# Kernel optimization log

Measured on AMD Instinct MI355X. Metric: run time of the kernel, lower is better.

Reference implementation:

```python
import jax, jax.numpy as jnp
import numpy as np
from jax import lax

# Norse default LIF/LI parameters with dt=0.001
DT_TAU_MEM = 0.1   # dt * tau_mem_inv (1/1e-2)
DT_TAU_SYN = 0.2   # dt * tau_syn_inv (1/5e-3)
V_TH = 0.5
ALPHA = 100.0      # SuperSpike surrogate slope (backward only)

@jax.custom_vjp
def spike(x):
    return (x > 0).astype(x.dtype)

def _spike_fwd(x):
    return (x > 0).astype(x.dtype), x

def _spike_bwd(x, g):
    # SuperSpike surrogate gradient: 1 / (alpha*|x| + 1)^2
    sg = 1.0 / (ALPHA * jnp.abs(x) + 1.0) ** 2
    return (g * sg,)

spike.defvjp(_spike_fwd, _spike_bwd)

def setup_inputs() -> dict:
    key = jax.random.key(0)
    k1, k2, k3 = jax.random.split(key, 3)
    T, B, C, H, W = 64, 512, 1, 28, 28
    IN, HID, OUT = 784, 2048, 10
    x = jax.random.normal(k1, (T, B, C, H, W), dtype=jnp.float32)
    # Kaiming-uniform-ish bias-free Linear weights, torch layout [out, in]
    w1 = jax.random.uniform(k2, (HID, IN), jnp.float32, -1.0, 1.0) / np.sqrt(IN)
    w_out = jax.random.uniform(k3, (OUT, HID), jnp.float32, -1.0, 1.0) / np.sqrt(HID)
    return {"x": x, "w1": w1, "w_out": w_out}

def reference(x, w1, w_out):
    T, B = x.shape[0], x.shape[1]
    HID, OUT = w1.shape[0], w_out.shape[0]
    xf = x.reshape(T, B, -1)  # [T, B, IN]

    def step(carry, xt):
        v1, i1, vo, io = carry
        cur = xt @ w1.T                       # fc1: [B, HID]
        # LIF: decay, threshold/spike/reset, then integrate new input current
        v1_dec = v1 + DT_TAU_MEM * (-v1 + i1)
        i1_dec = i1 * (1.0 - DT_TAU_SYN)
        z = spike(v1_dec - V_TH)
        v1_new = (1.0 - z) * v1_dec           # v_reset = 0
        i1_new = i1_dec + cur
        out_cur = z @ w_out.T                 # fc_out: [B, OUT]
        # LI readout: leaky integration (no spiking)
        vo_new = vo + DT_TAU_MEM * (-vo + io)
        io_new = io * (1.0 - DT_TAU_SYN) + out_cur
        return (v1_new, i1_new, vo_new, io_new), vo_new

    zh = jnp.zeros((B, HID), x.dtype)
    zo = jnp.zeros((B, OUT), x.dtype)
    _, voltages = lax.scan(step, (zh, zh, zo, zo), xf)  # [T, B, OUT]
    return jnp.max(voltages, axis=0)
```

## Files before the change

kernel.cpp:

```cpp
#include <hip/hip_runtime.h>
#include <cstdint>
#include <cstddef>

#define T_STEPS 64
#define BATCH 512
#define IN_F 784
#define KP 800
#define HID 2048
#define OUT_F 10

#define DEC_V 0.9f
#define DEC_I 0.8f
#define DT_V 0.1f
#define V_TH 0.5f

typedef __attribute__((ext_vector_type(8))) _Float16 f16x8;
typedef __attribute__((ext_vector_type(4))) float f32x4;

__device__ __forceinline__ void load_lds16(const _Float16* g, _Float16* l) {
  __builtin_amdgcn_global_load_lds(
      (const __attribute__((address_space(1))) void*)g,
      (__attribute__((address_space(3))) void*)l, 16, 0, 0);
}

__global__ __launch_bounds__(256)
void split_rows(const float* __restrict__ src, _Float16* __restrict__ hi,
                _Float16* __restrict__ lo) {
  const int row = blockIdx.x;
  for (int k = threadIdx.x; k < KP; k += 256) {
    float v = (k < IN_F) ? src[(size_t)row * IN_F + k] : 0.0f;
    _Float16 h = (_Float16)v;
    hi[(size_t)row * KP + k] = h;
    lo[(size_t)row * KP + k] = (_Float16)(v - (float)h);
  }
}

__global__ __launch_bounds__(256)
void pad_wo(const float* __restrict__ wo, _Float16* __restrict__ woF) {
  const int i = blockIdx.x * 256 + threadIdx.x;
  if (i >= 16 * HID) return;
  const int o = i / HID;
  woF[i] = (o < OUT_F) ? (_Float16)wo[i] : (_Float16)0.0f;
}

__global__ __launch_bounds__(256, 2)
void gemm_fc1(const _Float16* __restrict__ Ah, const _Float16* __restrict__ Al,
              const _Float16* __restrict__ Wh, const _Float16* __restrict__ Wl,
              float* __restrict__ C) {
  __shared__ _Float16 sAh[128 * 32];
  __shared__ _Float16 sAl[128 * 32];
  __shared__ _Float16 sWh[128 * 32];
  __shared__ _Float16 sWl[128 * 32];

  const int tid = threadIdx.x;
  const int lane = tid & 63;
  const int wv = tid >> 6;
  const int bn = blockIdx.x * 128;
  const int bm = blockIdx.y * 128;

  const int sr = (lane >> 2);
  const int skc = (lane & 3) * 8;

  const int wr = (wv >> 1) * 64;
  const int wc = (wv & 1) * 64;
  const int col = lane & 15;
  const int quad = lane >> 4;

  f32x4 acc[4][4] = {};

  const size_t arow = (size_t)(bm + wv * 32 + sr) * KP + skc;
  const size_t wrow = (size_t)(bn + wv * 32 + sr) * KP + skc;
  _Float16* const ldsbase = (_Float16*)((wv * 32 + sr * 0) , (void*)0) ;
  (void)ldsbase;

  for (int k0 = 0; k0 < KP; k0 += 32) {
    __syncthreads();
#pragma unroll
    for (int j = 0; j < 2; ++j) {
      const int ro = wv * 32 + j * 16;
      load_lds16(Ah + arow + (size_t)j * 16 * KP + k0, sAh + ro * 32);
      load_lds16(Al + arow + (size_t)j * 16 * KP + k0, sAl + ro * 32);
      load_lds16(Wh + wrow + (size_t)j * 16 * KP + k0, sWh + ro * 32);
      load_lds16(Wl + wrow + (size_t)j * 16 * KP + k0, sWl + ro * 32);
    }
    __syncthreads();

    f16x8 fah[4], fal[4], fwh[4], fwl[4];
#pragma unroll
    for (int i = 0; i < 4; ++i) {
      fah[i] = *(const f16x8*)&sAh[(wr + i * 16 + col) * 32 + quad * 8];
      fal[i] = *(const f16x8*)&sAl[(wr + i * 16 + col) * 32 + quad * 8];
      fwh[i] = *(const f16x8*)&sWh[(wc + i * 16 + col) * 32 + quad * 8];
      fwl[i] = *(const f16x8*)&sWl[(wc + i * 16 + col) * 32 + quad * 8];
    }
#pragma unroll
    for (int mi = 0; mi < 4; ++mi)
#pragma unroll
      for (int ni = 0; ni < 4; ++ni) {
        acc[mi][ni] = __builtin_amdgcn_mfma_f32_16x16x32_f16(fah[mi], fwh[ni], acc[mi][ni], 0, 0, 0);
        acc[mi][ni] = __builtin_amdgcn_mfma_f32_16x16x32_f16(fah[mi], fwl[ni], acc[mi][ni], 0, 0, 0);
        acc[mi][ni] = __builtin_amdgcn_mfma_f32_16x16x32_f16(fal[mi], fwh[ni], acc[mi][ni], 0, 0, 0);
      }
  }

#pragma unroll
  for (int mi = 0; mi < 4; ++mi)
#pragma unroll
    for (int ni = 0; ni < 4; ++ni)
#pragma unroll
      for (int r = 0; r < 4; ++r) {
        const int row = bm + wr + mi * 16 + quad * 4 + r;
        const int cg = bn + wc + ni * 16 + col;
        C[(size_t)row * HID + cg] = acc[mi][ni][r];
      }
}

__global__ __launch_bounds__(256)
void lif_scan(const float* __restrict__ cur, _Float16* __restrict__ zF,
              float* __restrict__ v1, float* __restrict__ i1, int tc) {
  const int idx = blockIdx.x * 256 + threadIdx.x;
  float v = v1[idx];
  float ci = i1[idx];
  for (int t = 0; t < tc; ++t) {
    const size_t off = (size_t)t * (BATCH * HID) + idx;
    float c = cur[off];
    float vd = DEC_V * v + DT_V * ci;
    float z = (vd > V_TH) ? 1.0f : 0.0f;
    v = (1.0f - z) * vd;
    ci = DEC_I * ci + c;
    zF[off] = (_Float16)z;
  }
  v1[idx] = v;
  i1[idx] = ci;
}

__global__ __launch_bounds__(256)
void out_proj(const _Float16* __restrict__ z, const _Float16* __restrict__ woF,
              float* __restrict__ outcur, int nrows) {
  const int wv = threadIdx.x >> 6;
  const int lane = threadIdx.x & 63;
  const int r0 = (blockIdx.x * 4 + wv) * 16;
  if (r0 >= nrows) return;
  const int col = lane & 15;
  const int quad = lane >> 4;
  const _Float16* zp = z + (size_t)(r0 + col) * HID + quad * 8;
  const _Float16* wp = woF + (size_t)col * HID + quad * 8;
  f32x4 acc = {};
#pragma unroll 8
  for (int k0 = 0; k0 < HID; k0 += 32) {
    f16x8 a = *(const f16x8*)(zp + k0);
    f16x8 b = *(const f16x8*)(wp + k0);
    acc = __builtin_amdgcn_mfma_f32_16x16x32_f16(a, b, acc, 0, 0, 0);
  }
  if (col < OUT_F) {
#pragma unroll
    for (int r = 0; r < 4; ++r)
      outcur[(size_t)(r0 + quad * 4 + r) * OUT_F + col] = acc[r];
  }
}

__global__ __launch_bounds__(256)
void li_scan(const float* __restrict__ outcur, float* __restrict__ out) {
  const int idx = blockIdx.x * 256 + threadIdx.x;
  if (idx >= BATCH * OUT_F) return;
  float vo = 0.f, io = 0.f, vmax = 0.f;
  for (int t = 0; t < T_STEPS; ++t) {
    float oc = outcur[(size_t)t * (BATCH * OUT_F) + idx];
    float von = DEC_V * vo + DT_V * io;
    io = DEC_I * io + oc;
    vo = von;
    vmax = fmaxf(vmax, von);
  }
  out[idx] = vmax;
}

__global__ void zero_state(float* __restrict__ p, int n) {
  int i = blockIdx.x * 256 + threadIdx.x;
  if (i < n) p[i] = 0.0f;
}

extern "C" void kernel_launch(void* const* d_in, const int* in_sizes, int n_in,
                              void* d_out, int out_size, void* d_ws, size_t ws_size,
                              hipStream_t stream) {
  const float* x  = (const float*)d_in[0];
  const float* w1 = (const float*)d_in[1];
  const float* wo = (const float*)d_in[2];
  float* out = (float*)d_out;

  const size_t BH = (size_t)BATCH * HID;

  float* v1 = (float*)d_ws;
  float* i1 = v1 + BH;
  float* outcur = i1 + BH;
  _Float16* WhG = (_Float16*)(outcur + (size_t)T_STEPS * BATCH * OUT_F);
  _Float16* WlG = WhG + (size_t)HID * KP;
  _Float16* woF = WlG + (size_t)HID * KP;
  char* chunk0 = (char*)(woF + 16 * HID);

  const size_t base_bytes = (size_t)(chunk0 - (char*)d_ws);
  const size_t per_step = BH * 4 + (size_t)2 * BATCH * KP * 2 + BH * 2;
  int Tc = 1;
  if (ws_size > base_bytes + per_step) {
    size_t m = (ws_size - base_bytes) / per_step;
    Tc = (m >= T_STEPS) ? T_STEPS : (int)m;
  }

  float* cur = (float*)chunk0;
  _Float16* AhC = (_Float16*)(cur + (size_t)Tc * BH);
  _Float16* AlC = AhC + (size_t)Tc * BATCH * KP;
  _Float16* zF  = AlC + (size_t)Tc * BATCH * KP;

  split_rows<<<HID, 256, 0, stream>>>(w1, WhG, WlG);
  pad_wo<<<(16 * HID + 255) / 256, 256, 0, stream>>>(wo, woF);
  zero_state<<<(int)((2 * BH + 255) / 256), 256, 0, stream>>>(v1, (int)(2 * BH));

  for (int t0 = 0; t0 < T_STEPS; t0 += Tc) {
    const int tc = (T_STEPS - t0 < Tc) ? (T_STEPS - t0) : Tc;
    const int nrows = tc * BATCH;
    split_rows<<<nrows, 256, 0, stream>>>(x + (size_t)t0 * BATCH * IN_F, AhC, AlC);
    dim3 grid(HID / 128, nrows / 128);
    gemm_fc1<<<grid, 256, 0, stream>>>(AhC, AlC, WhG, WlG, cur);
    lif_scan<<<(int)(BH / 256), 256, 0, stream>>>(cur, zF, v1, i1, tc);
    out_proj<<<(nrows + 63) / 64, 256, 0, stream>>>(
        zF, woF, outcur + (size_t)t0 * BATCH * OUT_F, nrows);
  }
  li_scan<<<(BATCH * OUT_F + 255) / 256, 256, 0, stream>>>(outcur, out);
}
```

Before: 667.3 us.

## Fuse LIF scan with output projection in LDS and vectorize input split

The separate LIF scan and out_proj kernels become one kernel. Each block handles one batch row and a 256-wide hidden chunk, keeps the spike history in LDS and does the 10-wide projection with MFMA there. Per-chunk partial sums are written to a buffer that li_scan reduces over the 8 chunks, which removes the global round-trip of the fp16 spike tensor and one launch per time chunk. split_rows now uses float4 loads with two rows per block, and gemm_fc1's launch bounds rise to 4 blocks per CU. The LDS spike array assumes tc ≤ 64, and the extra reduction adds a small amount of work.

```diff
diff --git a/kernel.cpp b/kernel.cpp
--- a/kernel.cpp
+++ b/kernel.cpp
@@ -15,6 +15,7 @@
 #define V_TH 0.5f
 
 typedef __attribute__((ext_vector_type(8))) _Float16 f16x8;
+typedef __attribute__((ext_vector_type(4))) _Float16 f16x4;
 typedef __attribute__((ext_vector_type(4))) float f32x4;
 
 __device__ __forceinline__ void load_lds16(const _Float16* g, _Float16* l) {
@@ -26,24 +27,25 @@
 __global__ __launch_bounds__(256)
 void split_rows(const float* __restrict__ src, _Float16* __restrict__ hi,
                 _Float16* __restrict__ lo) {
-  const int row = blockIdx.x;
-  for (int k = threadIdx.x; k < KP; k += 256) {
-    float v = (k < IN_F) ? src[(size_t)row * IN_F + k] : 0.0f;
-    _Float16 h = (_Float16)v;
-    hi[(size_t)row * KP + k] = h;
-    lo[(size_t)row * KP + k] = (_Float16)(v - (float)h);
-  }
-}
-
-__global__ __launch_bounds__(256)
-void pad_wo(const float* __restrict__ wo, _Float16* __restrict__ woF) {
-  const int i = blockIdx.x * 256 + threadIdx.x;
-  if (i >= 16 * HID) return;
-  const int o = i / HID;
-  woF[i] = (o < OUT_F) ? (_Float16)wo[i] : (_Float16)0.0f;
-}
-
-__global__ __launch_bounds__(256, 2)
+  const int row = blockIdx.x * 2 + (threadIdx.x >> 7);
+  const int ln = threadIdx.x & 127;
+  const float4* s = (const float4*)(src + (size_t)row * IN_F);
+#pragma unroll
+  for (int it = 0; it < 2; ++it) {
+    const int q = ln + it * 128;
+    if (q >= 200) break;
+    float4 v = (q < 196) ? s[q] : make_float4(0.f, 0.f, 0.f, 0.f);
+    f16x4 h, l;
+    h.x = (_Float16)v.x; l.x = (_Float16)(v.x - (float)h.x);
+    h.y = (_Float16)v.y; l.y = (_Float16)(v.y - (float)h.y);
+    h.z = (_Float16)v.z; l.z = (_Float16)(v.z - (float)h.z);
+    h.w = (_Float16)v.w; l.w = (_Float16)(v.w - (float)h.w);
+    *(f16x4*)&hi[(size_t)row * KP + q * 4] = h;
+    *(f16x4*)&lo[(size_t)row * KP + q * 4] = l;
+  }
+}
+
+__global__ __launch_bounds__(256, 4)
 void gemm_fc1(const _Float16* __restrict__ Ah, const _Float16* __restrict__ Al,
               const _Float16* __restrict__ Wh, const _Float16* __restrict__ Wl,
               float* __restrict__ C) {
@@ -58,7 +60,7 @@
   const int bn = blockIdx.x * 128;
   const int bm = blockIdx.y * 128;
 
-  const int sr = (lane >> 2);
+  const int sr = lane >> 2;
   const int skc = (lane & 3) * 8;
 
   const int wr = (wv >> 1) * 64;
@@ -70,8 +72,6 @@
 
   const size_t arow = (size_t)(bm + wv * 32 + sr) * KP + skc;
   const size_t wrow = (size_t)(bn + wv * 32 + sr) * KP + skc;
-  _Float16* const ldsbase = (_Float16*)((wv * 32 + sr * 0) , (void*)0) ;
-  (void)ldsbase;
 
   for (int k0 = 0; k0 < KP; k0 += 32) {
     __syncthreads();
@@ -116,57 +116,72 @@
 }
 
 __global__ __launch_bounds__(256)
-void lif_scan(const float* __restrict__ cur, _Float16* __restrict__ zF,
-              float* __restrict__ v1, float* __restrict__ i1, int tc) {
-  const int idx = blockIdx.x * 256 + threadIdx.x;
-  float v = v1[idx];
-  float ci = i1[idx];
+void lif_out(const float* __restrict__ cur, const float* __restrict__ wo,
+             float* __restrict__ v1, float* __restrict__ i1,
+             float* __restrict__ outP, int tc, int t0) {
+  __shared__ _Float16 zL[T_STEPS][264];
+  __shared__ _Float16 wT[16][264];
+
+  const int tid = threadIdx.x;
+  const int hc = blockIdx.x;
+  const int b = blockIdx.y;
+  const int hb = hc * 256;
+
+  for (int i = tid; i < 16 * 256; i += 256) {
+    const int n = i >> 8, k = i & 255;
+    wT[n][k] = (n < OUT_F) ? (_Float16)wo[(size_t)n * HID + hb + k] : (_Float16)0.f;
+  }
+
+  const int sidx = b * HID + hb + tid;
+  float v = v1[sidx];
+  float ci = i1[sidx];
+#pragma unroll 4
   for (int t = 0; t < tc; ++t) {
-    const size_t off = (size_t)t * (BATCH * HID) + idx;
-    float c = cur[off];
-    float vd = DEC_V * v + DT_V * ci;
-    float z = (vd > V_TH) ? 1.0f : 0.0f;
+    const float c = cur[(size_t)t * (BATCH * HID) + sidx];
+    const float vd = DEC_V * v + DT_V * ci;
+    const float z = (vd > V_TH) ? 1.0f : 0.0f;
     v = (1.0f - z) * vd;
     ci = DEC_I * ci + c;
-    zF[off] = (_Float16)z;
-  }
-  v1[idx] = v;
-  i1[idx] = ci;
-}
-
-__global__ __launch_bounds__(256)
-void out_proj(const _Float16* __restrict__ z, const _Float16* __restrict__ woF,
-              float* __restrict__ outcur, int nrows) {
-  const int wv = threadIdx.x >> 6;
-  const int lane = threadIdx.x & 63;
-  const int r0 = (blockIdx.x * 4 + wv) * 16;
-  if (r0 >= nrows) return;
+    zL[t][tid] = (_Float16)z;
+  }
+  v1[sidx] = v;
+  i1[sidx] = ci;
+  __syncthreads();
+
+  const int wv = tid >> 6;
+  const int lane = tid & 63;
   const int col = lane & 15;
   const int quad = lane >> 4;
-  const _Float16* zp = z + (size_t)(r0 + col) * HID + quad * 8;
-  const _Float16* wp = woF + (size_t)col * HID + quad * 8;
   f32x4 acc = {};
-#pragma unroll 8
-  for (int k0 = 0; k0 < HID; k0 += 32) {
-    f16x8 a = *(const f16x8*)(zp + k0);
-    f16x8 b = *(const f16x8*)(wp + k0);
-    acc = __builtin_amdgcn_mfma_f32_16x16x32_f16(a, b, acc, 0, 0, 0);
+  const _Float16* za = &zL[wv * 16 + col][0];
+  const _Float16* wb = &wT[col][0];
+#pragma unroll
+  for (int ks = 0; ks < 8; ++ks) {
+    f16x8 a = *(const f16x8*)(za + ks * 32 + quad * 8);
+    f16x8 bb = *(const f16x8*)(wb + ks * 32 + quad * 8);
+    acc = __builtin_amdgcn_mfma_f32_16x16x32_f16(a, bb, acc, 0, 0, 0);
   }
   if (col < OUT_F) {
 #pragma unroll
-    for (int r = 0; r < 4; ++r)
-      outcur[(size_t)(r0 + quad * 4 + r) * OUT_F + col] = acc[r];
+    for (int r = 0; r < 4; ++r) {
+      const int t = wv * 16 + quad * 4 + r;
+      if (t < tc)
+        outP[(((size_t)hc * T_STEPS + (t0 + t)) * BATCH + b) * OUT_F + col] = acc[r];
+    }
   }
 }
 
 __global__ __launch_bounds__(256)
-void li_scan(const float* __restrict__ outcur, float* __restrict__ out) {
+void li_scan(const float* __restrict__ outP, float* __restrict__ out) {
   const int idx = blockIdx.x * 256 + threadIdx.x;
   if (idx >= BATCH * OUT_F) return;
   float vo = 0.f, io = 0.f, vmax = 0.f;
   for (int t = 0; t < T_STEPS; ++t) {
-    float oc = outcur[(size_t)t * (BATCH * OUT_F) + idx];
-    float von = DEC_V * vo + DT_V * io;
+    float oc = 0.f;
+#pragma unroll
+    for (int hc = 0; hc < 8; ++hc)
+      oc += outP[((size_t)hc * T_STEPS + t) * (BATCH * OUT_F) + idx];
+    const float von = DEC_V * vo + DT_V * io;
     io = DEC_I * io + oc;
     vo = von;
     vmax = fmaxf(vmax, von);
@@ -191,14 +206,13 @@
 
   float* v1 = (float*)d_ws;
   float* i1 = v1 + BH;
-  float* outcur = i1 + BH;
-  _Float16* WhG = (_Float16*)(outcur + (size_t)T_STEPS * BATCH * OUT_F);
+  float* outP = i1 + BH;
+  _Float16* WhG = (_Float16*)(outP + (size_t)8 * T_STEPS * BATCH * OUT_F);
   _Float16* WlG = WhG + (size_t)HID * KP;
-  _Float16* woF = WlG + (size_t)HID * KP;
-  char* chunk0 = (char*)(woF + 16 * HID);
+  char* chunk0 = (char*)(WlG + (size_t)HID * KP);
 
   const size_t base_bytes = (size_t)(chunk0 - (char*)d_ws);
-  const size_t per_step = BH * 4 + (size_t)2 * BATCH * KP * 2 + BH * 2;
+  const size_t per_step = BH * 4 + (size_t)2 * BATCH * KP * 2;
   int Tc = 1;
   if (ws_size > base_bytes + per_step) {
     size_t m = (ws_size - base_bytes) / per_step;
@@ -208,21 +222,18 @@
   float* cur = (float*)chunk0;
   _Float16* AhC = (_Float16*)(cur + (size_t)Tc * BH);
   _Float16* AlC = AhC + (size_t)Tc * BATCH * KP;
-  _Float16* zF  = AlC + (size_t)Tc * BATCH * KP;
-
-  split_rows<<<HID, 256, 0, stream>>>(w1, WhG, WlG);
-  pad_wo<<<(16 * HID + 255) / 256, 256, 0, stream>>>(wo, woF);
+
+  split_rows<<<HID / 2, 256, 0, stream>>>(w1, WhG, WlG);
   zero_state<<<(int)((2 * BH + 255) / 256), 256, 0, stream>>>(v1, (int)(2 * BH));
 
   for (int t0 = 0; t0 < T_STEPS; t0 += Tc) {
     const int tc = (T_STEPS - t0 < Tc) ? (T_STEPS - t0) : Tc;
     const int nrows = tc * BATCH;
-    split_rows<<<nrows, 256, 0, stream>>>(x + (size_t)t0 * BATCH * IN_F, AhC, AlC);
+    split_rows<<<nrows / 2, 256, 0, stream>>>(x + (size_t)t0 * BATCH * IN_F, AhC, AlC);
     dim3 grid(HID / 128, nrows / 128);
     gemm_fc1<<<grid, 256, 0, stream>>>(AhC, AlC, WhG, WlG, cur);
-    lif_scan<<<(int)(BH / 256), 256, 0, stream>>>(cur, zF, v1, i1, tc);
-    out_proj<<<(nrows + 63) / 64, 256, 0, stream>>>(
-        zF, woF, outcur + (size_t)t0 * BATCH * OUT_F, nrows);
-  }
-  li_scan<<<(BATCH * OUT_F + 255) / 256, 256, 0, stream>>>(outcur, out);
-}
+    dim3 lgrid(HID / 256, BATCH);
+    lif_out<<<lgrid, 256, 0, stream>>>(cur, wo, v1, i1, outP, tc, t0);
+  }
+  li_scan<<<(BATCH * OUT_F + 255) / 256, 256, 0, stream>>>(outP, out);
+}
```

Measured after the change: 639.5 us. 4.2% less time.
